# Kernel tuning notes

Measured on AMD Instinct MI355X. Metric: run time of the kernel, lower is better.

Reference implementation:

```python
import jax, jax.numpy as jnp
import numpy as np

N_NODES = 100000
N_EDGES = 1600000
D_FEAT = 64
EPS = 1e-07


def setup_inputs() -> dict:
    key = jax.random.key(0)
    k1, k2, k3 = jax.random.split(key, 3)
    x = jax.random.normal(k1, (N_NODES, D_FEAT), dtype=jnp.float32)
    beta = jnp.ones((1,), dtype=jnp.float32)
    edge_row = jnp.sort(jax.random.randint(k2, (N_EDGES,), 0, N_NODES, dtype=jnp.int64))
    edge_col = jax.random.randint(k3, (N_EDGES,), 0, N_NODES, dtype=jnp.int64)
    return {"x": x, "beta": beta, "edge_row": edge_row, "edge_col": edge_col}


def reference(x, beta, edge_row, edge_col):
    # Gather endpoint features: [E, d]
    A = x[edge_row]
    B = x[edge_col]
    # Cosine similarity per edge, scaled by beta: [E]
    inner = jnp.sum(A * B, axis=1)
    norms = jnp.linalg.norm(A, axis=1) * jnp.linalg.norm(B, axis=1)
    sim = beta[0] * (inner / (norms + EPS))
    # Sparse row-wise softmax (tf.sparse.softmax): stable segment softmax over edges grouped by row
    row_max = jax.ops.segment_max(sim, edge_row, num_segments=N_NODES)
    e = jnp.exp(sim - row_max[edge_row])
    row_sum = jax.ops.segment_sum(e, edge_row, num_segments=N_NODES)
    p = e / row_sum[edge_row]  # [E]
    # SPMM: out[i] = sum_{(i,j) in E} p_ij * x[j]
    out = jax.ops.segment_sum(p[:, None] * B, edge_row, num_segments=N_NODES)
    return out
```

## Files before the change

kernel.cpp:

```cpp
#include <hip/hip_runtime.h>
#include <math.h>

#define D_FEAT 64
#define S_GET(v, i) ((v)[i])
typedef _Float16 v8h __attribute__((ext_vector_type(8)));
typedef float v4f __attribute__((ext_vector_type(4)));
typedef _Float16 h2 __attribute__((ext_vector_type(2)));

__device__ __forceinline__ v8h u2h8(uint4 u) { v8h v; __builtin_memcpy(&v, &u, 16); return v; }

__global__ __launch_bounds__(256)
void agnn_prep(const float* __restrict__ x, float* __restrict__ rn,
               uint2* __restrict__ xh, const int* __restrict__ edge_row,
               int* __restrict__ row_ptr, int n_nodes, int n_edges, int nb_prep) {
    if ((int)blockIdx.x < nb_prep) {
        int t = blockIdx.x * blockDim.x + threadIdx.x;
        int node = t >> 4;
        if (node >= n_nodes) return;
        int l4 = t & 15;
        float4 v = ((const float4*)x)[node * 16 + l4];
        float ss = v.x*v.x + v.y*v.y + v.z*v.z + v.w*v.w;
        #pragma unroll
        for (int off = 1; off < 16; off <<= 1) ss += __shfl_xor(ss, off, 64);
        if (l4 == 0) rn[node] = ss > 0.f ? rsqrtf(ss) : 0.f;
        h2 h0 = {(_Float16)v.x, (_Float16)v.y};
        h2 h1 = {(_Float16)v.z, (_Float16)v.w};
        uint2 u;
        __builtin_memcpy(&u.x, &h0, 4);
        __builtin_memcpy(&u.y, &h1, 4);
        xh[node * 16 + l4] = u;
    } else {
        int e = (blockIdx.x - nb_prep) * blockDim.x + threadIdx.x;
        if (e >= n_edges) return;
        int r1 = edge_row[e];
        int r0 = (e == 0) ? -1 : edge_row[e - 1];
        for (int r = r0 + 1; r <= r1; ++r) row_ptr[r] = e;
        if (e == n_edges - 1)
            for (int r = r1 + 1; r <= n_nodes; ++r) row_ptr[r] = n_edges;
    }
}

#define XCP_PITCH 144
#define P_PITCH    80
#define WAVE_LDS  (32 * XCP_PITCH + 16 * P_PITCH)

__global__ __launch_bounds__(256)
void agnn_fused(const float* __restrict__ beta_p,
                const int* __restrict__ edge_col,
                const int* __restrict__ edge_row,
                const int* __restrict__ row_ptr,
                const float* __restrict__ rn,
                const uint4* __restrict__ xh4,
                float* __restrict__ out, int n_nodes) {
    __shared__ char lds_raw[4 * WAVE_LDS];
    int wid  = threadIdx.x >> 6;
    int lane = threadIdx.x & 63;
    int q    = lane >> 4;
    int lo4  = lane & 15;
    char* XCP = lds_raw + wid * WAVE_LDS;
    char* PL  = XCP + 32 * XCP_PITCH;

    int tile = blockIdx.x * 4 + wid;
    int t0 = tile * 16;
    if (t0 >= n_nodes) return;

    int qnode = t0 + lo4; if (qnode >= n_nodes) qnode = n_nodes - 1;
    v8h a0 = u2h8(xh4[(size_t)qnode * 8 + q]);
    v8h a1 = u2h8(xh4[(size_t)qnode * 8 + 4 + q]);

    float beta  = beta_p[0];
    float shift = fabsf(beta);
    float4 rq = *(const float4*)(rn + t0 + q * 4);
    float brn0 = beta * rq.x, brn1 = beta * rq.y, brn2 = beta * rq.z, brn3 = beta * rq.w;

    int es   = row_ptr[t0];
    int tend = t0 + 16; if (tend > n_nodes) tend = n_nodes;
    int L    = row_ptr[tend] - es;

    v4f o0 = {0,0,0,0}, o1 = {0,0,0,0}, o2 = {0,0,0,0}, o3 = {0,0,0,0};
    float l0 = 0.f, l1 = 0.f, l2 = 0.f, l3 = 0.f;
    unsigned int selp = (lo4 & 1) ? 0x07060302u : 0x05040100u;
    int rbase = t0 + q * 4;

    for (int base = 0; base < L; base += 32) {
        int idx0 = base + lo4;
        bool cv0 = idx0 < L;
        int e0 = es + (cv0 ? idx0 : 0);
        int c0 = edge_col[e0];
        int rr0 = edge_row[e0];
        float rnc0 = rn[c0];
        uint4 u00 = xh4[(size_t)c0 * 8 + q];
        uint4 u01 = xh4[(size_t)c0 * 8 + 4 + q];
        int idx1 = base + 16 + lo4;
        bool cv1 = idx1 < L;
        int e1 = es + (cv1 ? idx1 : 0);
        int c1 = edge_col[e1];
        int rr1 = edge_row[e1];
        float rnc1 = rn[c1];
        uint4 u10 = xh4[(size_t)c1 * 8 + q];
        uint4 u11 = xh4[(size_t)c1 * 8 + 4 + q];

        v4f z0 = {0,0,0,0};
        z0 = __builtin_amdgcn_mfma_f32_16x16x32_f16(a0, u2h8(u00), z0, 0, 0, 0);
        z0 = __builtin_amdgcn_mfma_f32_16x16x32_f16(a1, u2h8(u01), z0, 0, 0, 0);
        v4f z1 = {0,0,0,0};
        z1 = __builtin_amdgcn_mfma_f32_16x16x32_f16(a0, u2h8(u10), z1, 0, 0, 0);
        z1 = __builtin_amdgcn_mfma_f32_16x16x32_f16(a1, u2h8(u11), z1, 0, 0, 0);

        {
            unsigned int colA = lo4 * 4, colB = (16 + lo4) * 4;
            char* pA = XCP + (4 * q) * XCP_PITCH;
            char* pB = XCP + (16 + 4 * q) * XCP_PITCH;
            *(unsigned int*)(pA + 0 * XCP_PITCH + colA) = u00.x;
            *(unsigned int*)(pA + 1 * XCP_PITCH + colA) = u00.y;
            *(unsigned int*)(pA + 2 * XCP_PITCH + colA) = u00.z;
            *(unsigned int*)(pA + 3 * XCP_PITCH + colA) = u00.w;
            *(unsigned int*)(pB + 0 * XCP_PITCH + colA) = u01.x;
            *(unsigned int*)(pB + 1 * XCP_PITCH + colA) = u01.y;
            *(unsigned int*)(pB + 2 * XCP_PITCH + colA) = u01.z;
            *(unsigned int*)(pB + 3 * XCP_PITCH + colA) = u01.w;
            *(unsigned int*)(pA + 0 * XCP_PITCH + colB) = u10.x;
            *(unsigned int*)(pA + 1 * XCP_PITCH + colB) = u10.y;
            *(unsigned int*)(pA + 2 * XCP_PITCH + colB) = u10.z;
            *(unsigned int*)(pA + 3 * XCP_PITCH + colB) = u10.w;
            *(unsigned int*)(pB + 0 * XCP_PITCH + colB) = u11.x;
            *(unsigned int*)(pB + 1 * XCP_PITCH + colB) = u11.y;
            *(unsigned int*)(pB + 2 * XCP_PITCH + colB) = u11.z;
            *(unsigned int*)(pB + 3 * XCP_PITCH + colB) = u11.w;
        }

        float w00 = (cv0 && rr0 == rbase + 0) ? __expf(brn0 * rnc0 * z0[0] - shift) : 0.f;
        float w01 = (cv0 && rr0 == rbase + 1) ? __expf(brn1 * rnc0 * z0[1] - shift) : 0.f;
        float w02 = (cv0 && rr0 == rbase + 2) ? __expf(brn2 * rnc0 * z0[2] - shift) : 0.f;
        float w03 = (cv0 && rr0 == rbase + 3) ? __expf(brn3 * rnc0 * z0[3] - shift) : 0.f;
        float w10 = (cv1 && rr1 == rbase + 0) ? __expf(brn0 * rnc1 * z1[0] - shift) : 0.f;
        float w11 = (cv1 && rr1 == rbase + 1) ? __expf(brn1 * rnc1 * z1[1] - shift) : 0.f;
        float w12 = (cv1 && rr1 == rbase + 2) ? __expf(brn2 * rnc1 * z1[2] - shift) : 0.f;
        float w13 = (cv1 && rr1 == rbase + 3) ? __expf(brn3 * rnc1 * z1[3] - shift) : 0.f;
        l0 += w00 + w10; l1 += w01 + w11; l2 += w02 + w12; l3 += w03 + w13;

        {
            unsigned int cA = lo4 * 2, cB = (16 + lo4) * 2;
            char* pm = PL + (q * 4) * P_PITCH;
            *(_Float16*)(pm + 0 * P_PITCH + cA) = (_Float16)w00;
            *(_Float16*)(pm + 1 * P_PITCH + cA) = (_Float16)w01;
            *(_Float16*)(pm + 2 * P_PITCH + cA) = (_Float16)w02;
            *(_Float16*)(pm + 3 * P_PITCH + cA) = (_Float16)w03;
            *(_Float16*)(pm + 0 * P_PITCH + cB) = (_Float16)w10;
            *(_Float16*)(pm + 1 * P_PITCH + cB) = (_Float16)w11;
            *(_Float16*)(pm + 2 * P_PITCH + cB) = (_Float16)w12;
            *(_Float16*)(pm + 3 * P_PITCH + cB) = (_Float16)w13;
        }

        v8h pah = u2h8(*(const uint4*)(PL + lo4 * P_PITCH + q * 16));
        {
            const char* rp = XCP + (0 + (lo4 >> 1)) * XCP_PITCH + q * 32;
            uint4 da = *(const uint4*)rp;
            uint4 db = *(const uint4*)(rp + 16);
            uint4 bb = { __builtin_amdgcn_perm(da.y, da.x, selp),
                         __builtin_amdgcn_perm(da.w, da.z, selp),
                         __builtin_amdgcn_perm(db.y, db.x, selp),
                         __builtin_amdgcn_perm(db.w, db.z, selp) };
            o0 = __builtin_amdgcn_mfma_f32_16x16x32_f16(pah, u2h8(bb), o0, 0, 0, 0);
        }
        {
            const char* rp = XCP + (8 + (lo4 >> 1)) * XCP_PITCH + q * 32;
            uint4 da = *(const uint4*)rp;
            uint4 db = *(const uint4*)(rp + 16);
            uint4 bb = { __builtin_amdgcn_perm(da.y, da.x, selp),
                         __builtin_amdgcn_perm(da.w, da.z, selp),
                         __builtin_amdgcn_perm(db.y, db.x, selp),
                         __builtin_amdgcn_perm(db.w, db.z, selp) };
            o1 = __builtin_amdgcn_mfma_f32_16x16x32_f16(pah, u2h8(bb), o1, 0, 0, 0);
        }
        {
            const char* rp = XCP + (16 + (lo4 >> 1)) * XCP_PITCH + q * 32;
            uint4 da = *(const uint4*)rp;
            uint4 db = *(const uint4*)(rp + 16);
            uint4 bb = { __builtin_amdgcn_perm(da.y, da.x, selp),
                         __builtin_amdgcn_perm(da.w, da.z, selp),
                         __builtin_amdgcn_perm(db.y, db.x, selp),
                         __builtin_amdgcn_perm(db.w, db.z, selp) };
            o2 = __builtin_amdgcn_mfma_f32_16x16x32_f16(pah, u2h8(bb), o2, 0, 0, 0);
        }
        {
            const char* rp = XCP + (24 + (lo4 >> 1)) * XCP_PITCH + q * 32;
            uint4 da = *(const uint4*)rp;
            uint4 db = *(const uint4*)(rp + 16);
            uint4 bb = { __builtin_amdgcn_perm(da.y, da.x, selp),
                         __builtin_amdgcn_perm(da.w, da.z, selp),
                         __builtin_amdgcn_perm(db.y, db.x, selp),
                         __builtin_amdgcn_perm(db.w, db.z, selp) };
            o3 = __builtin_amdgcn_mfma_f32_16x16x32_f16(pah, u2h8(bb), o3, 0, 0, 0);
        }
    }

    #pragma unroll
    for (int off = 1; off < 16; off <<= 1) {
        l0 += __shfl_xor(l0, off, 64);
        l1 += __shfl_xor(l1, off, 64);
        l2 += __shfl_xor(l2, off, 64);
        l3 += __shfl_xor(l3, off, 64);
    }
    float i0 = l0 > 0.f ? 1.f / l0 : 0.f;
    float i1 = l1 > 0.f ? 1.f / l1 : 0.f;
    float i2 = l2 > 0.f ? 1.f / l2 : 0.f;
    float i3 = l3 > 0.f ? 1.f / l3 : 0.f;

    int m0 = rbase;
    if (m0 + 0 < n_nodes) { float* p = out + (size_t)(m0 + 0) * 64 + lo4;
        p[0] = o0[0]*i0; p[16] = o1[0]*i0; p[32] = o2[0]*i0; p[48] = o3[0]*i0; }
    if (m0 + 1 < n_nodes) { float* p = out + (size_t)(m0 + 1) * 64 + lo4;
        p[0] = o0[1]*i1; p[16] = o1[1]*i1; p[32] = o2[1]*i1; p[48] = o3[1]*i1; }
    if (m0 + 2 < n_nodes) { float* p = out + (size_t)(m0 + 2) * 64 + lo4;
        p[0] = o0[2]*i2; p[16] = o1[2]*i2; p[32] = o2[2]*i2; p[48] = o3[2]*i2; }
    if (m0 + 3 < n_nodes) { float* p = out + (size_t)(m0 + 3) * 64 + lo4;
        p[0] = o0[3]*i3; p[16] = o1[3]*i3; p[32] = o2[3]*i3; p[48] = o3[3]*i3; }
}

extern "C" void kernel_launch(void* const* d_in, const int* in_sizes, int n_in,
                              void* d_out, int out_size, void* d_ws, size_t ws_size,
                              hipStream_t stream) {
    const float* x        = (const float*)d_in[0];
    const float* beta     = (const float*)d_in[1];
    const int*   edge_row = (const int*)d_in[2];
    const int*   edge_col = (const int*)d_in[3];
    float* out = (float*)d_out;

    int n_nodes = in_sizes[0] / D_FEAT;
    int n_edges = in_sizes[2];

    char* ws = (char*)d_ws;
    float* rn = (float*)ws;
    size_t off0 = ((size_t)n_nodes * sizeof(float) + 255) & ~(size_t)255;
    int* row_ptr = (int*)(ws + off0);
    size_t off1 = off0 + (((size_t)(n_nodes + 1) * sizeof(int) + 255) & ~(size_t)255);
    uint2* xh = (uint2*)(ws + off1);

    {
        int nb_prep = (n_nodes * 16 + 255) / 256;
        int nb_rp   = (n_edges + 255) / 256;
        agnn_prep<<<nb_prep + nb_rp, 256, 0, stream>>>(
            x, rn, xh, edge_row, row_ptr, n_nodes, n_edges, nb_prep);
    }
    {
        int tiles  = (n_nodes + 15) / 16;
        int blocks = (tiles + 3) / 4;
        agnn_fused<<<blocks, 256, 0, stream>>>(beta, edge_col, edge_row, row_ptr,
                                               rn, (const uint4*)xh, out, n_nodes);
    }
}
```

Baseline: 129.3 us.

## Software-pipeline edge gathers and replace edge_row loads with row_ptr bounds

Restructures the fused edge loop so that the column indices, norms and fp16 feature rows for the next 32-edge chunk are loaded while the current chunk's MFMAs, LDS staging and softmax weights run. Per-edge edge_row loads are removed; row membership is now tested against row_ptr offsets loaded once per lane. This hides gather latency and cuts global traffic. In exchange it raises register pressure from double-buffered uint4 operands, which could lower occupancy.

```diff
diff --git a/kernel.cpp b/kernel.cpp
--- a/kernel.cpp
+++ b/kernel.cpp
@@ -2,7 +2,6 @@
 #include <math.h>
 
 #define D_FEAT 64
-#define S_GET(v, i) ((v)[i])
 typedef _Float16 v8h __attribute__((ext_vector_type(8)));
 typedef float v4f __attribute__((ext_vector_type(4)));
 typedef _Float16 h2 __attribute__((ext_vector_type(2)));
@@ -47,7 +46,6 @@
 __global__ __launch_bounds__(256)
 void agnn_fused(const float* __restrict__ beta_p,
                 const int* __restrict__ edge_col,
-                const int* __restrict__ edge_row,
                 const int* __restrict__ row_ptr,
                 const float* __restrict__ rn,
                 const uint4* __restrict__ xh4,
@@ -70,128 +68,166 @@
 
     float beta  = beta_p[0];
     float shift = fabsf(beta);
-    float4 rq = *(const float4*)(rn + t0 + q * 4);
-    float brn0 = beta * rq.x, brn1 = beta * rq.y, brn2 = beta * rq.z, brn3 = beta * rq.w;
+    int rb = t0 + q * 4;
+    float brn0, brn1, brn2, brn3;
+    if (t0 + 16 <= n_nodes) {
+        float4 rq = *(const float4*)(rn + rb);
+        brn0 = beta * rq.x; brn1 = beta * rq.y; brn2 = beta * rq.z; brn3 = beta * rq.w;
+    } else {
+        brn0 = beta * rn[min(rb + 0, n_nodes - 1)];
+        brn1 = beta * rn[min(rb + 1, n_nodes - 1)];
+        brn2 = beta * rn[min(rb + 2, n_nodes - 1)];
+        brn3 = beta * rn[min(rb + 3, n_nodes - 1)];
+    }
 
     int es   = row_ptr[t0];
     int tend = t0 + 16; if (tend > n_nodes) tend = n_nodes;
     int L    = row_ptr[tend] - es;
 
+    int b0 = row_ptr[min(rb + 0, n_nodes)] - es;
+    int b1 = row_ptr[min(rb + 1, n_nodes)] - es;
+    int b2 = row_ptr[min(rb + 2, n_nodes)] - es;
+    int b3 = row_ptr[min(rb + 3, n_nodes)] - es;
+    int b4 = row_ptr[min(rb + 4, n_nodes)] - es;
+
     v4f o0 = {0,0,0,0}, o1 = {0,0,0,0}, o2 = {0,0,0,0}, o3 = {0,0,0,0};
     float l0 = 0.f, l1 = 0.f, l2 = 0.f, l3 = 0.f;
     unsigned int selp = (lo4 & 1) ? 0x07060302u : 0x05040100u;
-    int rbase = t0 + q * 4;
-
-    for (int base = 0; base < L; base += 32) {
-        int idx0 = base + lo4;
-        bool cv0 = idx0 < L;
-        int e0 = es + (cv0 ? idx0 : 0);
-        int c0 = edge_col[e0];
-        int rr0 = edge_row[e0];
-        float rnc0 = rn[c0];
-        uint4 u00 = xh4[(size_t)c0 * 8 + q];
-        uint4 u01 = xh4[(size_t)c0 * 8 + 4 + q];
-        int idx1 = base + 16 + lo4;
-        bool cv1 = idx1 < L;
-        int e1 = es + (cv1 ? idx1 : 0);
-        int c1 = edge_col[e1];
-        int rr1 = edge_row[e1];
-        float rnc1 = rn[c1];
-        uint4 u10 = xh4[(size_t)c1 * 8 + q];
-        uint4 u11 = xh4[(size_t)c1 * 8 + 4 + q];
-
-        v4f z0 = {0,0,0,0};
-        z0 = __builtin_amdgcn_mfma_f32_16x16x32_f16(a0, u2h8(u00), z0, 0, 0, 0);
-        z0 = __builtin_amdgcn_mfma_f32_16x16x32_f16(a1, u2h8(u01), z0, 0, 0, 0);
-        v4f z1 = {0,0,0,0};
-        z1 = __builtin_amdgcn_mfma_f32_16x16x32_f16(a0, u2h8(u10), z1, 0, 0, 0);
-        z1 = __builtin_amdgcn_mfma_f32_16x16x32_f16(a1, u2h8(u11), z1, 0, 0, 0);
-
+
+    int nch = (L + 31) >> 5;
+    if (nch > 0) {
+        int cc0, cc1;
         {
-            unsigned int colA = lo4 * 4, colB = (16 + lo4) * 4;
-            char* pA = XCP + (4 * q) * XCP_PITCH;
-            char* pB = XCP + (16 + 4 * q) * XCP_PITCH;
-            *(unsigned int*)(pA + 0 * XCP_PITCH + colA) = u00.x;
-            *(unsigned int*)(pA + 1 * XCP_PITCH + colA) = u00.y;
-            *(unsigned int*)(pA + 2 * XCP_PITCH + colA) = u00.z;
-            *(unsigned int*)(pA + 3 * XCP_PITCH + colA) = u00.w;
-            *(unsigned int*)(pB + 0 * XCP_PITCH + colA) = u01.x;
-            *(unsigned int*)(pB + 1 * XCP_PITCH + colA) = u01.y;
-            *(unsigned int*)(pB + 2 * XCP_PITCH + colA) = u01.z;
-            *(unsigned int*)(pB + 3 * XCP_PITCH + colA) = u01.w;
-            *(unsigned int*)(pA + 0 * XCP_PITCH + colB) = u10.x;
-            *(unsigned int*)(pA + 1 * XCP_PITCH + colB) = u10.y;
-            *(unsigned int*)(pA + 2 * XCP_PITCH + colB) = u10.z;
-            *(unsigned int*)(pA + 3 * XCP_PITCH + colB) = u10.w;
-            *(unsigned int*)(pB + 0 * XCP_PITCH + colB) = u11.x;
-            *(unsigned int*)(pB + 1 * XCP_PITCH + colB) = u11.y;
-            *(unsigned int*)(pB + 2 * XCP_PITCH + colB) = u11.z;
-            *(unsigned int*)(pB + 3 * XCP_PITCH + colB) = u11.w;
+            int i0 = lo4, i1 = lo4 + 16;
+            cc0 = edge_col[es + (i0 < L ? i0 : 0)];
+            cc1 = edge_col[es + (i1 < L ? i1 : 0)];
         }
-
-        float w00 = (cv0 && rr0 == rbase + 0) ? __expf(brn0 * rnc0 * z0[0] - shift) : 0.f;
-        float w01 = (cv0 && rr0 == rbase + 1) ? __expf(brn1 * rnc0 * z0[1] - shift) : 0.f;
-        float w02 = (cv0 && rr0 == rbase + 2) ? __expf(brn2 * rnc0 * z0[2] - shift) : 0.f;
-        float w03 = (cv0 && rr0 == rbase + 3) ? __expf(brn3 * rnc0 * z0[3] - shift) : 0.f;
-        float w10 = (cv1 && rr1 == rbase + 0) ? __expf(brn0 * rnc1 * z1[0] - shift) : 0.f;
-        float w11 = (cv1 && rr1 == rbase + 1) ? __expf(brn1 * rnc1 * z1[1] - shift) : 0.f;
-        float w12 = (cv1 && rr1 == rbase + 2) ? __expf(brn2 * rnc1 * z1[2] - shift) : 0.f;
-        float w13 = (cv1 && rr1 == rbase + 3) ? __expf(brn3 * rnc1 * z1[3] - shift) : 0.f;
-        l0 += w00 + w10; l1 += w01 + w11; l2 += w02 + w12; l3 += w03 + w13;
-
-        {
-            unsigned int cA = lo4 * 2, cB = (16 + lo4) * 2;
-            char* pm = PL + (q * 4) * P_PITCH;
-            *(_Float16*)(pm + 0 * P_PITCH + cA) = (_Float16)w00;
-            *(_Float16*)(pm + 1 * P_PITCH + cA) = (_Float16)w01;
-            *(_Float16*)(pm + 2 * P_PITCH + cA) = (_Float16)w02;
-            *(_Float16*)(pm + 3 * P_PITCH + cA) = (_Float16)w03;
-            *(_Float16*)(pm + 0 * P_PITCH + cB) = (_Float16)w10;
-            *(_Float16*)(pm + 1 * P_PITCH + cB) = (_Float16)w11;
-            *(_Float16*)(pm + 2 * P_PITCH + cB) = (_Float16)w12;
-            *(_Float16*)(pm + 3 * P_PITCH + cB) = (_Float16)w13;
-        }
-
-        v8h pah = u2h8(*(const uint4*)(PL + lo4 * P_PITCH + q * 16));
-        {
-            const char* rp = XCP + (0 + (lo4 >> 1)) * XCP_PITCH + q * 32;
-            uint4 da = *(const uint4*)rp;
-            uint4 db = *(const uint4*)(rp + 16);
-            uint4 bb = { __builtin_amdgcn_perm(da.y, da.x, selp),
-                         __builtin_amdgcn_perm(da.w, da.z, selp),
-                         __builtin_amdgcn_perm(db.y, db.x, selp),
-                         __builtin_amdgcn_perm(db.w, db.z, selp) };
-            o0 = __builtin_amdgcn_mfma_f32_16x16x32_f16(pah, u2h8(bb), o0, 0, 0, 0);
-        }
-        {
-            const char* rp = XCP + (8 + (lo4 >> 1)) * XCP_PITCH + q * 32;
-            uint4 da = *(const uint4*)rp;
-            uint4 db = *(const uint4*)(rp + 16);
-            uint4 bb = { __builtin_amdgcn_perm(da.y, da.x, selp),
-                         __builtin_amdgcn_perm(da.w, da.z, selp),
-                         __builtin_amdgcn_perm(db.y, db.x, selp),
-                         __builtin_amdgcn_perm(db.w, db.z, selp) };
-            o1 = __builtin_amdgcn_mfma_f32_16x16x32_f16(pah, u2h8(bb), o1, 0, 0, 0);
-        }
-        {
-            const char* rp = XCP + (16 + (lo4 >> 1)) * XCP_PITCH + q * 32;
-            uint4 da = *(const uint4*)rp;
-            uint4 db = *(const uint4*)(rp + 16);
-            uint4 bb = { __builtin_amdgcn_perm(da.y, da.x, selp),
-                         __builtin_amdgcn_perm(da.w, da.z, selp),
-                         __builtin_amdgcn_perm(db.y, db.x, selp),
-                         __builtin_amdgcn_perm(db.w, db.z, selp) };
-            o2 = __builtin_amdgcn_mfma_f32_16x16x32_f16(pah, u2h8(bb), o2, 0, 0, 0);
-        }
-        {
-            const char* rp = XCP + (24 + (lo4 >> 1)) * XCP_PITCH + q * 32;
-            uint4 da = *(const uint4*)rp;
-            uint4 db = *(const uint4*)(rp + 16);
-            uint4 bb = { __builtin_amdgcn_perm(da.y, da.x, selp),
-                         __builtin_amdgcn_perm(da.w, da.z, selp),
-                         __builtin_amdgcn_perm(db.y, db.x, selp),
-                         __builtin_amdgcn_perm(db.w, db.z, selp) };
-            o3 = __builtin_amdgcn_mfma_f32_16x16x32_f16(pah, u2h8(bb), o3, 0, 0, 0);
+        float rc0 = rn[cc0], rc1 = rn[cc1];
+        uint4 A00 = xh4[(size_t)cc0 * 8 + q];
+        uint4 A01 = xh4[(size_t)cc0 * 8 + 4 + q];
+        uint4 A10 = xh4[(size_t)cc1 * 8 + q];
+        uint4 A11 = xh4[(size_t)cc1 * 8 + 4 + q];
+
+        for (int ch = 0; ch < nch; ++ch) {
+            int base = ch << 5;
+            bool more = (ch + 1) < nch;
+
+            int nc0, nc1;
+            if (more) {
+                int i0 = base + 32 + lo4, i1 = i0 + 16;
+                nc0 = edge_col[es + (i0 < L ? i0 : 0)];
+                nc1 = edge_col[es + (i1 < L ? i1 : 0)];
+            } else { nc0 = cc0; nc1 = cc1; }
+
+            v4f z0 = {0,0,0,0};
+            z0 = __builtin_amdgcn_mfma_f32_16x16x32_f16(a0, u2h8(A00), z0, 0, 0, 0);
+            z0 = __builtin_amdgcn_mfma_f32_16x16x32_f16(a1, u2h8(A01), z0, 0, 0, 0);
+            v4f z1 = {0,0,0,0};
+            z1 = __builtin_amdgcn_mfma_f32_16x16x32_f16(a0, u2h8(A10), z1, 0, 0, 0);
+            z1 = __builtin_amdgcn_mfma_f32_16x16x32_f16(a1, u2h8(A11), z1, 0, 0, 0);
+
+            {
+                unsigned int colA = lo4 * 4, colB = (16 + lo4) * 4;
+                char* pA = XCP + (4 * q) * XCP_PITCH;
+                char* pB = XCP + (16 + 4 * q) * XCP_PITCH;
+                *(unsigned int*)(pA + 0 * XCP_PITCH + colA) = A00.x;
+                *(unsigned int*)(pA + 1 * XCP_PITCH + colA) = A00.y;
+                *(unsigned int*)(pA + 2 * XCP_PITCH + colA) = A00.z;
+                *(unsigned int*)(pA + 3 * XCP_PITCH + colA) = A00.w;
+                *(unsigned int*)(pB + 0 * XCP_PITCH + colA) = A01.x;
+                *(unsigned int*)(pB + 1 * XCP_PITCH + colA) = A01.y;
+                *(unsigned int*)(pB + 2 * XCP_PITCH + colA) = A01.z;
+                *(unsigned int*)(pB + 3 * XCP_PITCH + colA) = A01.w;
+                *(unsigned int*)(pA + 0 * XCP_PITCH + colB) = A10.x;
+                *(unsigned int*)(pA + 1 * XCP_PITCH + colB) = A10.y;
+                *(unsigned int*)(pA + 2 * XCP_PITCH + colB) = A10.z;
+                *(unsigned int*)(pA + 3 * XCP_PITCH + colB) = A10.w;
+                *(unsigned int*)(pB + 0 * XCP_PITCH + colB) = A11.x;
+                *(unsigned int*)(pB + 1 * XCP_PITCH + colB) = A11.y;
+                *(unsigned int*)(pB + 2 * XCP_PITCH + colB) = A11.z;
+                *(unsigned int*)(pB + 3 * XCP_PITCH + colB) = A11.w;
+            }
+
+            float nr0, nr1; uint4 B00, B01, B10, B11;
+            if (more) {
+                nr0 = rn[nc0]; nr1 = rn[nc1];
+                B00 = xh4[(size_t)nc0 * 8 + q];
+                B01 = xh4[(size_t)nc0 * 8 + 4 + q];
+                B10 = xh4[(size_t)nc1 * 8 + q];
+                B11 = xh4[(size_t)nc1 * 8 + 4 + q];
+            } else {
+                nr0 = rc0; nr1 = rc1;
+                B00 = A00; B01 = A01; B10 = A10; B11 = A11;
+            }
+
+            int i0g = base + lo4, i1g = i0g + 16;
+            float w00 = (i0g >= b0 && i0g < b1) ? __expf(brn0 * rc0 * z0[0] - shift) : 0.f;
+            float w01 = (i0g >= b1 && i0g < b2) ? __expf(brn1 * rc0 * z0[1] - shift) : 0.f;
+            float w02 = (i0g >= b2 && i0g < b3) ? __expf(brn2 * rc0 * z0[2] - shift) : 0.f;
+            float w03 = (i0g >= b3 && i0g < b4) ? __expf(brn3 * rc0 * z0[3] - shift) : 0.f;
+            float w10 = (i1g >= b0 && i1g < b1) ? __expf(brn0 * rc1 * z1[0] - shift) : 0.f;
+            float w11 = (i1g >= b1 && i1g < b2) ? __expf(brn1 * rc1 * z1[1] - shift) : 0.f;
+            float w12 = (i1g >= b2 && i1g < b3) ? __expf(brn2 * rc1 * z1[2] - shift) : 0.f;
+            float w13 = (i1g >= b3 && i1g < b4) ? __expf(brn3 * rc1 * z1[3] - shift) : 0.f;
+            l0 += w00 + w10; l1 += w01 + w11; l2 += w02 + w12; l3 += w03 + w13;
+
+            {
+                unsigned int cA = lo4 * 2, cB = (16 + lo4) * 2;
+                char* pm = PL + (q * 4) * P_PITCH;
+                *(_Float16*)(pm + 0 * P_PITCH + cA) = (_Float16)w00;
+                *(_Float16*)(pm + 1 * P_PITCH + cA) = (_Float16)w01;
+                *(_Float16*)(pm + 2 * P_PITCH + cA) = (_Float16)w02;
+                *(_Float16*)(pm + 3 * P_PITCH + cA) = (_Float16)w03;
+                *(_Float16*)(pm + 0 * P_PITCH + cB) = (_Float16)w10;
+                *(_Float16*)(pm + 1 * P_PITCH + cB) = (_Float16)w11;
+                *(_Float16*)(pm + 2 * P_PITCH + cB) = (_Float16)w12;
+                *(_Float16*)(pm + 3 * P_PITCH + cB) = (_Float16)w13;
+            }
+
+            v8h pah = u2h8(*(const uint4*)(PL + lo4 * P_PITCH + q * 16));
+            {
+                const char* rp = XCP + (0 + (lo4 >> 1)) * XCP_PITCH + q * 32;
+                uint4 da = *(const uint4*)rp;
+                uint4 db = *(const uint4*)(rp + 16);
+                uint4 bb = { __builtin_amdgcn_perm(da.y, da.x, selp),
+                             __builtin_amdgcn_perm(da.w, da.z, selp),
+                             __builtin_amdgcn_perm(db.y, db.x, selp),
+                             __builtin_amdgcn_perm(db.w, db.z, selp) };
+                o0 = __builtin_amdgcn_mfma_f32_16x16x32_f16(pah, u2h8(bb), o0, 0, 0, 0);
+            }
+            {
+                const char* rp = XCP + (8 + (lo4 >> 1)) * XCP_PITCH + q * 32;
+                uint4 da = *(const uint4*)rp;
+                uint4 db = *(const uint4*)(rp + 16);
+                uint4 bb = { __builtin_amdgcn_perm(da.y, da.x, selp),
+                             __builtin_amdgcn_perm(da.w, da.z, selp),
+                             __builtin_amdgcn_perm(db.y, db.x, selp),
+                             __builtin_amdgcn_perm(db.w, db.z, selp) };
+                o1 = __builtin_amdgcn_mfma_f32_16x16x32_f16(pah, u2h8(bb), o1, 0, 0, 0);
+            }
+            {
+                const char* rp = XCP + (16 + (lo4 >> 1)) * XCP_PITCH + q * 32;
+                uint4 da = *(const uint4*)rp;
+                uint4 db = *(const uint4*)(rp + 16);
+                uint4 bb = { __builtin_amdgcn_perm(da.y, da.x, selp),
+                             __builtin_amdgcn_perm(da.w, da.z, selp),
+                             __builtin_amdgcn_perm(db.y, db.x, selp),
+                             __builtin_amdgcn_perm(db.w, db.z, selp) };
+                o2 = __builtin_amdgcn_mfma_f32_16x16x32_f16(pah, u2h8(bb), o2, 0, 0, 0);
+            }
+            {
+                const char* rp = XCP + (24 + (lo4 >> 1)) * XCP_PITCH + q * 32;
+                uint4 da = *(const uint4*)rp;
+                uint4 db = *(const uint4*)(rp + 16);
+                uint4 bb = { __builtin_amdgcn_perm(da.y, da.x, selp),
+                             __builtin_amdgcn_perm(da.w, da.z, selp),
+                             __builtin_amdgcn_perm(db.y, db.x, selp),
+                             __builtin_amdgcn_perm(db.w, db.z, selp) };
+                o3 = __builtin_amdgcn_mfma_f32_16x16x32_f16(pah, u2h8(bb), o3, 0, 0, 0);
+            }
+
+            cc0 = nc0; cc1 = nc1; rc0 = nr0; rc1 = nr1;
+            A00 = B00; A01 = B01; A10 = B10; A11 = B11;
         }
     }
 
@@ -207,7 +243,7 @@
     float i2 = l2 > 0.f ? 1.f / l2 : 0.f;
     float i3 = l3 > 0.f ? 1.f / l3 : 0.f;
 
-    int m0 = rbase;
+    int m0 = rb;
     if (m0 + 0 < n_nodes) { float* p = out + (size_t)(m0 + 0) * 64 + lo4;
         p[0] = o0[0]*i0; p[16] = o1[0]*i0; p[32] = o2[0]*i0; p[48] = o3[0]*i0; }
     if (m0 + 1 < n_nodes) { float* p = out + (size_t)(m0 + 1) * 64 + lo4;
@@ -246,7 +282,7 @@
     {
         int tiles  = (n_nodes + 15) / 16;
         int blocks = (tiles + 3) / 4;
-        agnn_fused<<<blocks, 256, 0, stream>>>(beta, edge_col, edge_row, row_ptr,
+        agnn_fused<<<blocks, 256, 0, stream>>>(beta, edge_col, row_ptr,
                                                rn, (const uint4*)xh, out, n_nodes);
     }
 }
```

Measured after the change: 127.9 us. About the same (-1.1%).
